# Kernel optimization log

Hardware: AMD Instinct MI355X
Metric: run time of the kernel (lower is better)

## Reference

```python
import jax, jax.numpy as jnp
import numpy as np

N_NODES = 100000
N_EDGES = 1600000
F_IN = 128
HIDDEN = 128
N_CLASSES = 2
N_GRAPHS = 512


def setup_inputs() -> dict:
    key = jax.random.key(0)
    ks = jax.random.split(key, 10)
    node_features = jax.random.normal(ks[0], (N_NODES, F_IN), dtype=jnp.float32)
    edge_index = jax.random.randint(ks[1], (2, N_EDGES), 0, N_NODES, dtype=jnp.int64)
    batch = jnp.sort(jax.random.randint(ks[2], (N_NODES,), 0, N_GRAPHS, dtype=jnp.int64))
    s1 = 1.0 / np.sqrt(F_IN)
    s2 = 1.0 / np.sqrt(HIDDEN)
    W1 = jax.random.uniform(ks[3], (F_IN, HIDDEN), jnp.float32, -s1, s1)
    b1 = jnp.zeros((HIDDEN,), jnp.float32)
    W2 = jax.random.uniform(ks[4], (HIDDEN, HIDDEN), jnp.float32, -s2, s2)
    b2 = jnp.zeros((HIDDEN,), jnp.float32)
    Wlin = jax.random.uniform(ks[5], (HIDDEN, N_CLASSES), jnp.float32, -s2, s2)
    blin = jax.random.uniform(ks[6], (N_CLASSES,), jnp.float32, -s2, s2)
    return {"node_features": node_features, "edge_index": edge_index, "batch": batch,
            "W1": W1, "b1": b1, "W2": W2, "b2": b2, "Wlin": Wlin, "blin": blin}


def _gcn_conv(x, src, dst, norm, W, b, n_nodes):
    # transform-then-propagate (PyG GCNConv default)
    h = x @ W                                   # [N, H]
    msg = h[src] * norm[:, None]                # gather + edge scale
    out = jax.ops.segment_sum(msg, dst, num_segments=n_nodes)  # scatter-add
    return out + b


def reference(node_features, edge_index, batch, W1, b1, W2, b2, Wlin, blin):
    n = node_features.shape[0]
    loop = jnp.arange(n, dtype=edge_index.dtype)
    src = jnp.concatenate([edge_index[0], loop])  # add self-loops
    dst = jnp.concatenate([edge_index[1], loop])
    # symmetric degree normalization: deg counts incoming edges incl. self-loop
    deg = jax.ops.segment_sum(jnp.ones_like(src, dtype=node_features.dtype), dst, num_segments=n)
    dis = jnp.where(deg > 0, jax.lax.rsqrt(jnp.maximum(deg, 1.0)), 0.0)
    norm = dis[src] * dis[dst]

    x = jax.nn.relu(_gcn_conv(node_features, src, dst, norm, W1, b1, n))
    x = jax.nn.relu(_gcn_conv(x, src, dst, norm, W2, b2, n))

    # global mean pool over graphs
    ones = jnp.ones((n,), dtype=x.dtype)
    counts = jax.ops.segment_sum(ones, batch, num_segments=N_GRAPHS)
    sums = jax.ops.segment_sum(x, batch, num_segments=N_GRAPHS)
    pooled = sums / jnp.maximum(counts, 1.0)[:, None]

    # dropout is identity in eval mode
    return pooled @ Wlin + blin
```

## Files before the change

kernel.cpp:

```cpp
#include <hip/hip_runtime.h>
#include <hip/hip_bf16.h>
#include <hip/hip_fp16.h>

constexpr int NN = 100000;
constexpr int NE = 1600000;
constexpr int NG = 512;
constexpr int F  = 128;

constexpr int NB   = 392;
constexpr int RCAP = 4608;
constexpr int CAP  = 32;
constexpr int NCH  = 8;

typedef _Float16 f16;
typedef f16 f16x2 __attribute__((ext_vector_type(2)));
typedef f16 f16x4 __attribute__((ext_vector_type(4)));
typedef f16 f16x8 __attribute__((ext_vector_type(8)));
typedef float f32x4 __attribute__((ext_vector_type(4)));
typedef unsigned int u32;
typedef u32 u32x4a __attribute__((ext_vector_type(4), aligned(4)));

__global__ void init_cursors(int* __restrict__ gcur) {
    int b = blockIdx.x * blockDim.x + threadIdx.x;
    if (b < NB) gcur[b] = b * RCAP;
}

__global__ __launch_bounds__(256) void bin_edges(const int* __restrict__ ei,
                                                 int* __restrict__ gcur,
                                                 u32* __restrict__ binned) {
    __shared__ u32 stage[NB][CAP];
    __shared__ int scnt[NB];
    for (int b = threadIdx.x; b < NB; b += 256) scnt[b] = 0;
    __syncthreads();
    const int per = NE / 256;
    const int e0 = blockIdx.x * per;
    for (int r = 0; r < per; r += 256) {
        int k = r + threadIdx.x;
        if (k < per) {
            int e = e0 + k;
            int s = ei[e], d = ei[NE + e];
            int b = d >> 8;
            u32 v = ((u32)(d & 255) << 24) | (u32)s;
            int p = atomicAdd(&scnt[b], 1);
            if (p < CAP) stage[b][p] = v;
        }
        __syncthreads();
        for (int b2 = threadIdx.x; b2 < NB; b2 += 256) {
            int n = scnt[b2];
            if (n >= 16) {
                int f = n & ~15;
                int base = atomicAdd(&gcur[b2], f);
                const u32x4a* st4 = (const u32x4a*)&stage[b2][0];
                u32x4a* out4 = (u32x4a*)&binned[base];
                for (int j = 0; j < (f >> 2); j++) out4[j] = st4[j];
                for (int j = 0; j < n - f; j++) stage[b2][j] = stage[b2][f + j];
                scnt[b2] = n - f;
            }
        }
        __syncthreads();
    }
    for (int b2 = threadIdx.x; b2 < NB; b2 += 256) {
        int n = scnt[b2];
        if (n > 0) {
            int base = atomicAdd(&gcur[b2], n);
            for (int j = 0; j < n; j++) binned[base + j] = stage[b2][j];
        }
    }
}

__global__ void scan_buckets(const int* __restrict__ gcur, int* __restrict__ bucketBase,
                             int* __restrict__ offs) {
    __shared__ int tmp[512];
    int t = threadIdx.x;
    int c = (t < NB) ? (gcur[t] - t * RCAP) : 0;
    tmp[t] = c;
    __syncthreads();
    for (int d = 1; d < 512; d <<= 1) {
        int x = (t >= d) ? tmp[t - d] : 0;
        __syncthreads();
        tmp[t] += x;
        __syncthreads();
    }
    if (t < NB) bucketBase[t] = tmp[t] - c;
    if (t == 0) offs[NN] = NE;
}

__global__ __launch_bounds__(256) void build_csr(const u32* __restrict__ binned,
                                                 const int* __restrict__ gcur,
                                                 const int* __restrict__ bucketBase,
                                                 int* __restrict__ offs,
                                                 float* __restrict__ dis,
                                                 int* __restrict__ csr_src) {
    __shared__ u32 ed[RCAP];
    __shared__ u32 lcsr[RCAP];
    __shared__ int hist[256];
    __shared__ int loff[256];
    __shared__ int lcur[256];
    const int b = blockIdx.x;
    int cnt = gcur[b] - b * RCAP;
    if (cnt > RCAP) cnt = RCAP;
    const int gbase = bucketBase[b];
    const int t = threadIdx.x;
    hist[t] = 0;
    __syncthreads();
    for (int j = t; j < cnt; j += 256) {
        u32 v = binned[(size_t)b * RCAP + j];
        ed[j] = v;
        atomicAdd(&hist[v >> 24], 1);
    }
    __syncthreads();
    int h = hist[t];
    loff[t] = h;
    __syncthreads();
    for (int d = 1; d < 256; d <<= 1) {
        int x = (t >= d) ? loff[t - d] : 0;
        __syncthreads();
        loff[t] += x;
        __syncthreads();
    }
    int excl = loff[t] - h;
    lcur[t] = excl;
    int node = (b << 8) + t;
    if (node < NN) {
        offs[node] = gbase + excl;
        dis[node] = rsqrtf((float)(h + 1));
    }
    __syncthreads();
    for (int j = t; j < cnt; j += 256) {
        u32 v = ed[j];
        int p = atomicAdd(&lcur[v >> 24], 1);
        lcsr[p] = v & 0x1FFFFu;
    }
    __syncthreads();
    for (int j = t; j < cnt; j += 256) csr_src[gbase + j] = (int)lcsr[j];
}

__global__ void prep_w(const float* __restrict__ W1, const float* __restrict__ W2,
                       f16* __restrict__ WT1, f16* __restrict__ WT2) {
    int idx = blockIdx.x * blockDim.x + threadIdx.x;
    if (idx < 128 * 128) {
        int n = idx >> 7, k = idx & 127;
        WT1[idx] = (f16)W1[k * 128 + n];
        WT2[idx] = (f16)W2[k * 128 + n];
    }
}

template<bool IN_HALF>
__global__ __launch_bounds__(256) void gemm_mfma(const void* __restrict__ Xv,
                                                 const f16* __restrict__ WT,
                                                 const float* __restrict__ dis,
                                                 f16* __restrict__ H, int M) {
    __shared__ f16 sX[128 * 136];
    __shared__ f16 sW[128 * 136];
    const int tid = threadIdx.x;
    const int row0 = blockIdx.x * 128;
    {
        const f16x8* Wg = (const f16x8*)WT;
        #pragma unroll
        for (int i = 0; i < 8; i++) {
            int idx = tid + 256 * i;
            int n = idx >> 4, kc = idx & 15;
            *(f16x8*)&sW[n * 136 + kc * 8] = Wg[idx];
        }
    }
    if (IN_HALF) {
        const f16x8* Xg = (const f16x8*)Xv;
        #pragma unroll
        for (int i = 0; i < 8; i++) {
            int idx = tid + 256 * i;
            int r = idx >> 4, kc = idx & 15;
            f16x8 v = {};
            if (row0 + r < M) v = Xg[(size_t)(row0 + r) * 16 + kc];
            *(f16x8*)&sX[r * 136 + kc * 8] = v;
        }
    } else {
        const float4* Xg = (const float4*)Xv;
        #pragma unroll
        for (int i = 0; i < 16; i++) {
            int idx = tid + 256 * i;
            int r = idx >> 5, c4 = idx & 31;
            float4 v = make_float4(0.f, 0.f, 0.f, 0.f);
            if (row0 + r < M) v = Xg[(size_t)(row0 + r) * 32 + c4];
            f16x4 hv = {(f16)v.x, (f16)v.y, (f16)v.z, (f16)v.w};
            *(f16x4*)&sX[r * 136 + c4 * 4] = hv;
        }
    }
    __syncthreads();

    const int wid = tid >> 6;
    const int lane = tid & 63;
    const int wrow = wid * 32;
    const int lr = lane & 15;
    const int lk = (lane >> 4) * 8;
    f32x4 acc[2][8] = {};
    #pragma unroll
    for (int ks = 0; ks < 4; ks++) {
        f16x8 a[2], b[8];
        #pragma unroll
        for (int mf = 0; mf < 2; mf++)
            a[mf] = *(const f16x8*)&sX[(wrow + mf * 16 + lr) * 136 + ks * 32 + lk];
        #pragma unroll
        for (int nf = 0; nf < 8; nf++)
            b[nf] = *(const f16x8*)&sW[(nf * 16 + lr) * 136 + ks * 32 + lk];
        #pragma unroll
        for (int mf = 0; mf < 2; mf++)
            #pragma unroll
            for (int nf = 0; nf < 8; nf++)
                acc[mf][nf] = __builtin_amdgcn_mfma_f32_16x16x32_f16(a[mf], b[nf], acc[mf][nf], 0, 0, 0);
    }
    const int crow = (lane >> 4) * 4;
    #pragma unroll
    for (int mf = 0; mf < 2; mf++) {
        #pragma unroll
        for (int reg = 0; reg < 4; reg++) {
            int row = row0 + wrow + mf * 16 + crow + reg;
            if (row < M) {
                float sc = dis[row];
                #pragma unroll
                for (int nf = 0; nf < 8; nf++)
                    H[(size_t)row * 128 + nf * 16 + lr] = (f16)(acc[mf][nf][reg] * sc);
            }
        }
    }
}

__global__ __launch_bounds__(256) void aggregate16(const f16* __restrict__ h,
                                                   const int* __restrict__ offs,
                                                   const int* __restrict__ csr_src,
                                                   const float* __restrict__ dis,
                                                   const float* __restrict__ bias,
                                                   f16* __restrict__ out, int n) {
    int i = blockIdx.x * 4 + (threadIdx.x >> 6);
    if (i >= n) return;
    const int lane = threadIdx.x & 63;
    const int q = lane >> 4;
    const int r = lane & 15;
    float acc[8] = {};
    if (q == 0) {
        f16x8 v = *(const f16x8*)(h + (size_t)i * F + r * 8);
        #pragma unroll
        for (int j = 0; j < 8; j++) acc[j] = (float)v[j];
    }
    const int s = offs[i], e = offs[i + 1];
    int t = s + q;
    for (; t + 4 < e; t += 8) {
        int sr0 = csr_src[t];
        int sr1 = csr_src[t + 4];
        f16x8 v0 = *(const f16x8*)(h + (size_t)sr0 * F + r * 8);
        f16x8 v1 = *(const f16x8*)(h + (size_t)sr1 * F + r * 8);
        #pragma unroll
        for (int j = 0; j < 8; j++) acc[j] += (float)v0[j] + (float)v1[j];
    }
    if (t < e) {
        int sr = csr_src[t];
        f16x8 v = *(const f16x8*)(h + (size_t)sr * F + r * 8);
        #pragma unroll
        for (int j = 0; j < 8; j++) acc[j] += (float)v[j];
    }
    #pragma unroll
    for (int j = 0; j < 8; j++) {
        acc[j] += __shfl_xor(acc[j], 16);
        acc[j] += __shfl_xor(acc[j], 32);
    }
    if (q == 0) {
        float di = dis[i];
        const float4* b4 = (const float4*)bias;
        float4 bb0 = b4[r * 2], bb1 = b4[r * 2 + 1];
        float bb[8] = {bb0.x, bb0.y, bb0.z, bb0.w, bb1.x, bb1.y, bb1.z, bb1.w};
        f16x8 o;
        #pragma unroll
        for (int j = 0; j < 8; j++) {
            float v = fmaf(acc[j], di, bb[j]);
            o[j] = (f16)(v > 0.f ? v : 0.f);
        }
        *(f16x8*)(out + (size_t)i * F + r * 8) = o;
    }
}

__global__ __launch_bounds__(256) void pool_partial(const f16* __restrict__ x,
                                                    const int* __restrict__ batch,
                                                    float* __restrict__ partial, int n) {
    int g = blockIdx.x;
    __shared__ int se[2];
    if (threadIdx.x < 2) {
        int target = g + threadIdx.x;
        int lo = 0, hi = n;
        while (lo < hi) {
            int mid = (lo + hi) >> 1;
            if (batch[mid] < target) lo = mid + 1; else hi = mid;
        }
        se[threadIdx.x] = lo;
    }
    __syncthreads();
    int s = se[0], e = se[1];
    int wid = threadIdx.x >> 6, lane = threadIdx.x & 63;
    int slot = blockIdx.y * 4 + wid;
    float a0 = 0.f, a1 = 0.f;
    const f16x2* x2 = (const f16x2*)x;
    for (int i = s + slot; i < e; i += 4 * NCH) {
        f16x2 v = x2[(size_t)i * 64 + lane];
        a0 += (float)v[0];
        a1 += (float)v[1];
    }
    __shared__ float red[4][128];
    red[wid][lane * 2] = a0;
    red[wid][lane * 2 + 1] = a1;
    __syncthreads();
    if (wid == 0) {
        float s0 = red[0][lane * 2] + red[1][lane * 2] + red[2][lane * 2] + red[3][lane * 2];
        float s1 = red[0][lane * 2 + 1] + red[1][lane * 2 + 1] + red[2][lane * 2 + 1] + red[3][lane * 2 + 1];
        float2* pp = (float2*)&partial[((size_t)g * NCH + blockIdx.y) * F];
        pp[lane] = make_float2(s0, s1);
    }
}

__global__ __launch_bounds__(128) void pool_final(const float* __restrict__ partial,
                                                  const int* __restrict__ batch,
                                                  const float* __restrict__ Wlin,
                                                  const float* __restrict__ blin,
                                                  float* __restrict__ out, int n) {
    int g = blockIdx.x;
    int f = threadIdx.x;
    __shared__ int se[2];
    if (threadIdx.x < 2) {
        int target = g + threadIdx.x;
        int lo = 0, hi = n;
        while (lo < hi) {
            int mid = (lo + hi) >> 1;
            if (batch[mid] < target) lo = mid + 1; else hi = mid;
        }
        se[threadIdx.x] = lo;
    }
    __syncthreads();
    int s = se[0], e = se[1];
    float acc = 0.f;
    #pragma unroll
    for (int c = 0; c < NCH; c++) acc += partial[((size_t)g * NCH + c) * F + f];
    float cnt = (float)((e - s) > 0 ? (e - s) : 1);
    float p = acc / cnt;
    float v0 = p * Wlin[f * 2 + 0];
    float v1 = p * Wlin[f * 2 + 1];
    #pragma unroll
    for (int o = 32; o > 0; o >>= 1) {
        v0 += __shfl_xor(v0, o);
        v1 += __shfl_xor(v1, o);
    }
    __shared__ float red[4];
    int wid = threadIdx.x >> 6;
    if ((threadIdx.x & 63) == 0) { red[wid * 2] = v0; red[wid * 2 + 1] = v1; }
    __syncthreads();
    if (threadIdx.x == 0) {
        out[g * 2 + 0] = red[0] + red[2] + blin[0];
        out[g * 2 + 1] = red[1] + red[3] + blin[1];
    }
}

extern "C" void kernel_launch(void* const* d_in, const int* in_sizes, int n_in,
                              void* d_out, int out_size, void* d_ws, size_t ws_size,
                              hipStream_t stream) {
    const float* X     = (const float*)d_in[0];
    const int*   ei    = (const int*)d_in[1];
    const int*   batch = (const int*)d_in[2];
    const float* W1    = (const float*)d_in[3];
    const float* b1    = (const float*)d_in[4];
    const float* W2    = (const float*)d_in[5];
    const float* b2    = (const float*)d_in[6];
    const float* Wlin  = (const float*)d_in[7];
    const float* blin  = (const float*)d_in[8];
    float* out = (float*)d_out;

    char* p = (char*)d_ws;
    auto alloc = [&](size_t bytes) -> char* {
        char* r = p;
        p += (bytes + 255) & ~size_t(255);
        return r;
    };
    int*   gcur       = (int*)alloc((size_t)NB * 4);
    int*   bucketBase = (int*)alloc((size_t)NB * 4);
    int*   offs       = (int*)alloc((size_t)(NN + 1) * 4);
    float* dis        = (float*)alloc((size_t)NN * 4);
    u32*   binned     = (u32*)alloc((size_t)NB * RCAP * 4);
    int*   csr_src    = (int*)alloc((size_t)NE * 4);
    f16*   WT1        = (f16*)alloc((size_t)128 * 128 * 2);
    f16*   WT2        = (f16*)alloc((size_t)128 * 128 * 2);
    f16*   bufA       = (f16*)alloc((size_t)NN * F * 2);
    f16*   bufB       = (f16*)alloc((size_t)NN * F * 2);
    float* partial    = (float*)alloc((size_t)NG * NCH * F * 4);

    init_cursors<<<2, 256, 0, stream>>>(gcur);
    bin_edges<<<256, 256, 0, stream>>>(ei, gcur, binned);
    scan_buckets<<<1, 512, 0, stream>>>(gcur, bucketBase, offs);
    build_csr<<<NB, 256, 0, stream>>>(binned, gcur, bucketBase, offs, dis, csr_src);
    prep_w<<<64, 256, 0, stream>>>(W1, W2, WT1, WT2);

    gemm_mfma<false><<<(NN + 127) / 128, 256, 0, stream>>>(X, WT1, dis, bufA, NN);
    aggregate16<<<(NN + 3) / 4, 256, 0, stream>>>(bufA, offs, csr_src, dis, b1, bufB, NN);
    gemm_mfma<true><<<(NN + 127) / 128, 256, 0, stream>>>(bufB, WT2, dis, bufA, NN);
    aggregate16<<<(NN + 3) / 4, 256, 0, stream>>>(bufA, offs, csr_src, dis, b2, bufB, NN);
    pool_partial<<<dim3(NG, NCH), 256, 0, stream>>>(bufB, batch, partial, NN);
    pool_final<<<NG, 128, 0, stream>>>(partial, batch, Wlin, blin, out, NN);
}
```

Before: 264.9 us.

## Merge init into prep_w, widen binning grid, direct-load GEMM, unroll gather

Folds cursor initialisation into the weight-prep kernel to save a launch, and doubles the number of binning blocks. Adds nontemporal loads for edge, binned and CSR index streams. Replaces the LDS-staged MFMA GEMM with one that loads A and B fragments straight from global memory. Unrolls the neighbour gather to four rows per step for more loads in flight. Direct global loads remove the LDS staging and barrier, but W is reread by every wave and the loads become strided.

```diff
diff --git a/kernel.cpp b/kernel.cpp
--- a/kernel.cpp
+++ b/kernel.cpp
@@ -11,6 +11,7 @@
 constexpr int RCAP = 4608;
 constexpr int CAP  = 32;
 constexpr int NCH  = 8;
+constexpr int BINB = 512;
 
 typedef _Float16 f16;
 typedef f16 f16x2 __attribute__((ext_vector_type(2)));
@@ -20,9 +21,16 @@
 typedef unsigned int u32;
 typedef u32 u32x4a __attribute__((ext_vector_type(4), aligned(4)));
 
-__global__ void init_cursors(int* __restrict__ gcur) {
-    int b = blockIdx.x * blockDim.x + threadIdx.x;
-    if (b < NB) gcur[b] = b * RCAP;
+__global__ void prep_w(const float* __restrict__ W1, const float* __restrict__ W2,
+                       f16* __restrict__ WT1, f16* __restrict__ WT2,
+                       int* __restrict__ gcur) {
+    int idx = blockIdx.x * blockDim.x + threadIdx.x;
+    if (idx < NB) gcur[idx] = idx * RCAP;
+    if (idx < 128 * 128) {
+        int n = idx >> 7, k = idx & 127;
+        WT1[idx] = (f16)W1[k * 128 + n];
+        WT2[idx] = (f16)W2[k * 128 + n];
+    }
 }
 
 __global__ __launch_bounds__(256) void bin_edges(const int* __restrict__ ei,
@@ -32,13 +40,14 @@
     __shared__ int scnt[NB];
     for (int b = threadIdx.x; b < NB; b += 256) scnt[b] = 0;
     __syncthreads();
-    const int per = NE / 256;
+    const int per = NE / BINB;
     const int e0 = blockIdx.x * per;
     for (int r = 0; r < per; r += 256) {
         int k = r + threadIdx.x;
         if (k < per) {
             int e = e0 + k;
-            int s = ei[e], d = ei[NE + e];
+            int s = __builtin_nontemporal_load(&ei[e]);
+            int d = __builtin_nontemporal_load(&ei[NE + e]);
             int b = d >> 8;
             u32 v = ((u32)(d & 255) << 24) | (u32)s;
             int p = atomicAdd(&scnt[b], 1);
@@ -104,7 +113,7 @@
     hist[t] = 0;
     __syncthreads();
     for (int j = t; j < cnt; j += 256) {
-        u32 v = binned[(size_t)b * RCAP + j];
+        u32 v = __builtin_nontemporal_load(&binned[(size_t)b * RCAP + j]);
         ed[j] = v;
         atomicAdd(&hist[v >> 24], 1);
     }
@@ -135,60 +144,15 @@
     for (int j = t; j < cnt; j += 256) csr_src[gbase + j] = (int)lcsr[j];
 }
 
-__global__ void prep_w(const float* __restrict__ W1, const float* __restrict__ W2,
-                       f16* __restrict__ WT1, f16* __restrict__ WT2) {
-    int idx = blockIdx.x * blockDim.x + threadIdx.x;
-    if (idx < 128 * 128) {
-        int n = idx >> 7, k = idx & 127;
-        WT1[idx] = (f16)W1[k * 128 + n];
-        WT2[idx] = (f16)W2[k * 128 + n];
-    }
-}
-
 template<bool IN_HALF>
-__global__ __launch_bounds__(256) void gemm_mfma(const void* __restrict__ Xv,
-                                                 const f16* __restrict__ WT,
-                                                 const float* __restrict__ dis,
-                                                 f16* __restrict__ H, int M) {
-    __shared__ f16 sX[128 * 136];
-    __shared__ f16 sW[128 * 136];
+__global__ __launch_bounds__(256) void gemm_direct(const void* __restrict__ Xv,
+                                                   const f16* __restrict__ WT,
+                                                   const float* __restrict__ dis,
+                                                   f16* __restrict__ H, int M) {
     const int tid = threadIdx.x;
-    const int row0 = blockIdx.x * 128;
-    {
-        const f16x8* Wg = (const f16x8*)WT;
-        #pragma unroll
-        for (int i = 0; i < 8; i++) {
-            int idx = tid + 256 * i;
-            int n = idx >> 4, kc = idx & 15;
-            *(f16x8*)&sW[n * 136 + kc * 8] = Wg[idx];
-        }
-    }
-    if (IN_HALF) {
-        const f16x8* Xg = (const f16x8*)Xv;
-        #pragma unroll
-        for (int i = 0; i < 8; i++) {
-            int idx = tid + 256 * i;
-            int r = idx >> 4, kc = idx & 15;
-            f16x8 v = {};
-            if (row0 + r < M) v = Xg[(size_t)(row0 + r) * 16 + kc];
-            *(f16x8*)&sX[r * 136 + kc * 8] = v;
-        }
-    } else {
-        const float4* Xg = (const float4*)Xv;
-        #pragma unroll
-        for (int i = 0; i < 16; i++) {
-            int idx = tid + 256 * i;
-            int r = idx >> 5, c4 = idx & 31;
-            float4 v = make_float4(0.f, 0.f, 0.f, 0.f);
-            if (row0 + r < M) v = Xg[(size_t)(row0 + r) * 32 + c4];
-            f16x4 hv = {(f16)v.x, (f16)v.y, (f16)v.z, (f16)v.w};
-            *(f16x4*)&sX[r * 136 + c4 * 4] = hv;
-        }
-    }
-    __syncthreads();
-
     const int wid = tid >> 6;
     const int lane = tid & 63;
+    const int row0 = blockIdx.x * 128;
     const int wrow = wid * 32;
     const int lr = lane & 15;
     const int lk = (lane >> 4) * 8;
@@ -197,11 +161,22 @@
     for (int ks = 0; ks < 4; ks++) {
         f16x8 a[2], b[8];
         #pragma unroll
-        for (int mf = 0; mf < 2; mf++)
-            a[mf] = *(const f16x8*)&sX[(wrow + mf * 16 + lr) * 136 + ks * 32 + lk];
+        for (int mf = 0; mf < 2; mf++) {
+            int row = row0 + wrow + mf * 16 + lr;
+            row = row < M ? row : M - 1;
+            if (IN_HALF) {
+                a[mf] = *(const f16x8*)((const f16*)Xv + (size_t)row * 128 + ks * 32 + lk);
+            } else {
+                const float* Xf = (const float*)Xv + (size_t)row * 128 + ks * 32 + lk;
+                float4 v0 = *(const float4*)Xf;
+                float4 v1 = *(const float4*)(Xf + 4);
+                a[mf] = f16x8{(f16)v0.x, (f16)v0.y, (f16)v0.z, (f16)v0.w,
+                              (f16)v1.x, (f16)v1.y, (f16)v1.z, (f16)v1.w};
+            }
+        }
         #pragma unroll
         for (int nf = 0; nf < 8; nf++)
-            b[nf] = *(const f16x8*)&sW[(nf * 16 + lr) * 136 + ks * 32 + lk];
+            b[nf] = *(const f16x8*)(WT + (size_t)(nf * 16 + lr) * 128 + ks * 32 + lk);
         #pragma unroll
         for (int mf = 0; mf < 2; mf++)
             #pragma unroll
@@ -221,6 +196,43 @@
                     H[(size_t)row * 128 + nf * 16 + lr] = (f16)(acc[mf][nf][reg] * sc);
             }
         }
+    }
+}
+
+__device__ __forceinline__ void gather_rows(const f16* __restrict__ h, int i,
+                                            const int* __restrict__ offs,
+                                            const int* __restrict__ csr_src,
+                                            int q, int r, float acc[8]) {
+    if (q == 0) {
+        f16x8 v = *(const f16x8*)(h + (size_t)i * F + r * 8);
+        #pragma unroll
+        for (int j = 0; j < 8; j++) acc[j] = (float)v[j];
+    }
+    const int s = offs[i], e = offs[i + 1];
+    int t = s + q;
+    for (; t + 12 < e; t += 16) {
+        int sr0 = __builtin_nontemporal_load(&csr_src[t]);
+        int sr1 = __builtin_nontemporal_load(&csr_src[t + 4]);
+        int sr2 = __builtin_nontemporal_load(&csr_src[t + 8]);
+        int sr3 = __builtin_nontemporal_load(&csr_src[t + 12]);
+        f16x8 v0 = *(const f16x8*)(h + (size_t)sr0 * F + r * 8);
+        f16x8 v1 = *(const f16x8*)(h + (size_t)sr1 * F + r * 8);
+        f16x8 v2 = *(const f16x8*)(h + (size_t)sr2 * F + r * 8);
+        f16x8 v3 = *(const f16x8*)(h + (size_t)sr3 * F + r * 8);
+        #pragma unroll
+        for (int j = 0; j < 8; j++)
+            acc[j] += ((float)v0[j] + (float)v1[j]) + ((float)v2[j] + (float)v3[j]);
+    }
+    for (; t < e; t += 4) {
+        int sr = __builtin_nontemporal_load(&csr_src[t]);
+        f16x8 v = *(const f16x8*)(h + (size_t)sr * F + r * 8);
+        #pragma unroll
+        for (int j = 0; j < 8; j++) acc[j] += (float)v[j];
+    }
+    #pragma unroll
+    for (int j = 0; j < 8; j++) {
+        acc[j] += __shfl_xor(acc[j], 16);
+        acc[j] += __shfl_xor(acc[j], 32);
     }
 }
 
@@ -236,32 +248,7 @@
     const int q = lane >> 4;
     const int r = lane & 15;
     float acc[8] = {};
-    if (q == 0) {
-        f16x8 v = *(const f16x8*)(h + (size_t)i * F + r * 8);
-        #pragma unroll
-        for (int j = 0; j < 8; j++) acc[j] = (float)v[j];
-    }
-    const int s = offs[i], e = offs[i + 1];
-    int t = s + q;
-    for (; t + 4 < e; t += 8) {
-        int sr0 = csr_src[t];
-        int sr1 = csr_src[t + 4];
-        f16x8 v0 = *(const f16x8*)(h + (size_t)sr0 * F + r * 8);
-        f16x8 v1 = *(const f16x8*)(h + (size_t)sr1 * F + r * 8);
-        #pragma unroll
-        for (int j = 0; j < 8; j++) acc[j] += (float)v0[j] + (float)v1[j];
-    }
-    if (t < e) {
-        int sr = csr_src[t];
-        f16x8 v = *(const f16x8*)(h + (size_t)sr * F + r * 8);
-        #pragma unroll
-        for (int j = 0; j < 8; j++) acc[j] += (float)v[j];
-    }
-    #pragma unroll
-    for (int j = 0; j < 8; j++) {
-        acc[j] += __shfl_xor(acc[j], 16);
-        acc[j] += __shfl_xor(acc[j], 32);
-    }
+    gather_rows(h, i, offs, csr_src, q, r, acc);
     if (q == 0) {
         float di = dis[i];
         const float4* b4 = (const float4*)bias;
@@ -387,15 +374,14 @@
     f16*   bufB       = (f16*)alloc((size_t)NN * F * 2);
     float* partial    = (float*)alloc((size_t)NG * NCH * F * 4);
 
-    init_cursors<<<2, 256, 0, stream>>>(gcur);
-    bin_edges<<<256, 256, 0, stream>>>(ei, gcur, binned);
+    prep_w<<<64, 256, 0, stream>>>(W1, W2, WT1, WT2, gcur);
+    bin_edges<<<BINB, 256, 0, stream>>>(ei, gcur, binned);
     scan_buckets<<<1, 512, 0, stream>>>(gcur, bucketBase, offs);
     build_csr<<<NB, 256, 0, stream>>>(binned, gcur, bucketBase, offs, dis, csr_src);
-    prep_w<<<64, 256, 0, stream>>>(W1, W2, WT1, WT2);
-
-    gemm_mfma<false><<<(NN + 127) / 128, 256, 0, stream>>>(X, WT1, dis, bufA, NN);
+
+    gemm_direct<false><<<(NN + 127) / 128, 256, 0, stream>>>(X, WT1, dis, bufA, NN);
     aggregate16<<<(NN + 3) / 4, 256, 0, stream>>>(bufA, offs, csr_src, dis, b1, bufB, NN);
-    gemm_mfma<true><<<(NN + 127) / 128, 256, 0, stream>>>(bufB, WT2, dis, bufA, NN);
+    gemm_direct<true><<<(NN + 127) / 128, 256, 0, stream>>>(bufB, WT2, dis, bufA, NN);
     aggregate16<<<(NN + 3) / 4, 256, 0, stream>>>(bufA, offs, csr_src, dis, b2, bufB, NN);
     pool_partial<<<dim3(NG, NCH), 256, 0, stream>>>(bufB, batch, partial, NN);
     pool_final<<<NG, 128, 0, stream>>>(partial, batch, Wlin, blin, out, NN);
```

Result: slower. 273.1 us (+3.1%).
